# Kernel optimization log

Hardware: AMD Instinct MI355X
Metric: run time of the kernel (lower is better)

Reference implementation:

```python
import jax, jax.numpy as jnp
import numpy as np

EMBED_DIM = 512
NUM_HEADS = 8
HEAD_DIM = EMBED_DIM // NUM_HEADS
EDGE_DIM = 16
B, N = 2, 2048


def setup_inputs() -> dict:
    key = jax.random.key(0)
    ks = jax.random.split(key, 16)
    s = 1.0 / np.sqrt(EMBED_DIM)
    inp = {
        "x": jax.random.normal(ks[0], (B, N, EMBED_DIM), dtype=jnp.float32),
        "adjacency": jax.random.uniform(ks[1], (B, N, N), dtype=jnp.float32),
        # torch.nn.Linear stores weight as (out, in); we keep that convention
        "Wq": jax.random.uniform(ks[2], (EMBED_DIM, EMBED_DIM), minval=-s, maxval=s),
        "bq": jax.random.uniform(ks[3], (EMBED_DIM,), minval=-s, maxval=s),
        "Wk": jax.random.uniform(ks[4], (EMBED_DIM, EMBED_DIM), minval=-s, maxval=s),
        "bk": jax.random.uniform(ks[5], (EMBED_DIM,), minval=-s, maxval=s),
        "Wv": jax.random.uniform(ks[6], (EMBED_DIM, EMBED_DIM), minval=-s, maxval=s),
        "bv": jax.random.uniform(ks[7], (EMBED_DIM,), minval=-s, maxval=s),
        "Wo": jax.random.uniform(ks[8], (EMBED_DIM, EMBED_DIM), minval=-s, maxval=s),
        "bo": jax.random.uniform(ks[9], (EMBED_DIM,), minval=-s, maxval=s),
        # edge MLP: Linear(1 -> edge_dim) then Linear(edge_dim -> num_heads)
        "We1": jax.random.uniform(ks[10], (EDGE_DIM, 1), minval=-1.0, maxval=1.0),
        "be1": jax.random.uniform(ks[11], (EDGE_DIM,), minval=-1.0, maxval=1.0),
        "We2": jax.random.uniform(ks[12], (NUM_HEADS, EDGE_DIM), minval=-0.25, maxval=0.25),
        "be2": jax.random.uniform(ks[13], (NUM_HEADS,), minval=-0.25, maxval=0.25),
        "edge_bias": jnp.zeros((NUM_HEADS,), dtype=jnp.float32),
    }
    return inp


def reference(x, adjacency, Wq, bq, Wk, bk, Wv, bv, Wo, bo, We1, be1, We2, be2, edge_bias):
    b, n, _ = x.shape
    scale = HEAD_DIM ** (-0.5)

    def split_heads(t):  # (b, n, E) -> (b, H, n, d)
        return t.reshape(b, n, NUM_HEADS, HEAD_DIM).transpose(0, 2, 1, 3)

    q = split_heads(x @ Wq.T + bq)
    k = split_heads(x @ Wk.T + bk)
    v = split_heads(x @ Wv.T + bv)

    # (b, H, n, n)
    attn_scores = jnp.einsum('bhid,bhjd->bhij', q, k) * scale

    # edge MLP applied pointwise to each adjacency entry: 1 -> edge_dim -> num_heads
    # hidden: (b, n, n, edge_dim)
    hidden = jax.nn.relu(adjacency[..., None] * We1[:, 0] + be1)
    edge_attn = jnp.einsum('bijE,hE->bhij', hidden, We2) + be2[None, :, None, None]

    boost = adjacency[:, None, :, :] * edge_bias[None, :, None, None]
    attn_scores = attn_scores + edge_attn + boost

    attn_probs = jax.nn.softmax(attn_scores, axis=-1)
    out = jnp.einsum('bhij,bhjd->bhid', attn_probs, v)
    out = out.transpose(0, 2, 1, 3).reshape(b, n, EMBED_DIM)
    out = out @ Wo.T + bo
    return out
```

## Files before the change

### kernel.cpp

```cpp
#include <hip/hip_runtime.h>
#include <stdint.h>


#define SEQ 2048
#define EMB 512
#define NH  8
#define HD  64
#define NB  2
#define L2E 1.4426950408889634f

typedef unsigned int   u32;
typedef unsigned short u16;
typedef u32   u32x4  __attribute__((ext_vector_type(4)));
typedef float f32x4  __attribute__((ext_vector_type(4)));
typedef __bf16 bf16x8 __attribute__((ext_vector_type(8)));

#define MFMA16(a, b, c) __builtin_amdgcn_mfma_f32_16x16x32_bf16((a), (b), (c), 0, 0, 0)

static __device__ __forceinline__ u16 f2bf(float f) {
  return __builtin_bit_cast(u16, (__bf16)f);
}
static __device__ __forceinline__ u32 pack2(float a, float b) {
  return (u32)f2bf(a) | ((u32)f2bf(b) << 16);
}
static __device__ __forceinline__ bf16x8 ldfrag(const u16* p) {
  return __builtin_bit_cast(bf16x8, *(const u32x4*)p);
}


__global__ void prep_kernel(const float* __restrict__ x,
                            const float* __restrict__ Wq, const float* __restrict__ Wk,
                            const float* __restrict__ Wv, const float* __restrict__ Wo,
                            const float* __restrict__ We1, const float* __restrict__ be1,
                            const float* __restrict__ We2, const float* __restrict__ be2,
                            const float* __restrict__ ebias,
                            u16* __restrict__ xb, u16* __restrict__ wqkv,
                            u16* __restrict__ wob, float* __restrict__ co) {
  const int blk = blockIdx.x, tid = threadIdx.x;
  if (blk < 2048) {
    int i = (blk * 256 + tid) * 4;
    float4 v = *(const float4*)(x + i);
    *(uint2*)(xb + i) = make_uint2(pack2(v.x, v.y), pack2(v.z, v.w));
  } else if (blk < 3072) {
    int i = ((blk - 2048) * 256 + tid) * 4;
    int m = i >> 18;
    int off = i & 262143;
    const float* src = (m == 0) ? Wq : ((m == 1) ? Wk : ((m == 2) ? Wv : Wo));
    u16* dst = (m < 3) ? (wqkv + (size_t)m * 262144) : wob;
    float4 v = *(const float4*)(src + off);
    *(uint2*)(dst + off) = make_uint2(pack2(v.x, v.y), pack2(v.z, v.w));
  } else {
    const int e = tid & 15, h = tid >> 4;
    if (tid < 128) {
      co[49 + e * 8 + h] = 0.0f;
      if (h == 0) { co[17 + e] = 0.0f; co[33 + e] = 0.0f; }
    }
    __syncthreads();
    if (tid < 128) {
      float w1 = We1[e], b1 = be1[e], w2 = We2[h * 16 + e];
      float u0 = b1, u1 = w1 + b1;
      bool on  = (u0 >= 0.0f) && (u1 >= 0.0f);
      bool off = (u0 <= 0.0f) && (u1 <= 0.0f);
      bool crossing = (!on) && (!off);
      float ca = on ? (w2 * b1) : (crossing ? 0.5f * w2 * b1 : 0.0f);
      float cb = on ? (w2 * w1) : (crossing ? 0.5f * w2 * w1 : 0.0f);
      #pragma unroll
      for (int d = 1; d < 16; d <<= 1) { ca += __shfl_xor(ca, d); cb += __shfl_xor(cb, d); }
      if (e == 0) { co[h] = (be2[h] + ca) * L2E; co[8 + h] = (ebias[h] + cb) * L2E; }
      unsigned long long msk = __ballot(crossing);
      int midx = __popcll(msk & 0xFFFFull & ((1ull << e) - 1ull));
      int mcnt = __popcll(msk & 0xFFFFull);
      if (crossing) {
        co[49 + midx * 8 + h] = 0.5f * w2 * L2E;
        if (h == 0) { co[17 + midx] = w1; co[33 + midx] = b1; }
      }
      if (tid == 0) ((int*)co)[16] = mcnt;
    }
  }
}

#define LDA 40
__global__ __launch_bounds__(256) void gemm_qkv_kernel(
    const u16* __restrict__ A, const u16* __restrict__ Bm,
    const float* __restrict__ bq, const float* __restrict__ bk, const float* __restrict__ bv,
    u16* __restrict__ qh, u16* __restrict__ ksw, u16* __restrict__ vsw)
{
  __shared__ u16 As[64 * LDA];
  __shared__ u16 Bs[128 * LDA];
  const int tid = threadIdx.x;
  const int lane = tid & 63, w = tid >> 6;
  const int q = lane >> 4, l15 = lane & 15;
  const int m0 = blockIdx.y * 64;
  const int n0 = blockIdx.x * 128;

  f32x4 acc[4][2];
  f32x4 zero = {0.f, 0.f, 0.f, 0.f};
  #pragma unroll
  for (int i = 0; i < 4; i++) { acc[i][0] = zero; acc[i][1] = zero; }

  const bool isA = tid < 128;
  const int arow = tid >> 1, ahalf = tid & 1;
  const int brow = tid - 128;
  const u16* ga = A  + (size_t)(m0 + arow) * EMB + ahalf * 16;
  const u16* gb = Bm + (size_t)(n0 + brow) * EMB;
  u16* la = &As[arow * LDA + ahalf * 16];
  u16* lb = &Bs[brow * LDA];

  u32x4 p0, p1, p2, p3;
  if (isA) {
    p0 = *(const u32x4*)(ga); p1 = *(const u32x4*)(ga + 8); ga += 32;
  } else {
    p0 = *(const u32x4*)(gb);      p1 = *(const u32x4*)(gb + 8);
    p2 = *(const u32x4*)(gb + 16); p3 = *(const u32x4*)(gb + 24); gb += 32;
  }

  for (int k0 = 0; k0 < EMB; k0 += 32) {
    __syncthreads();
    if (isA) { *(u32x4*)(la) = p0; *(u32x4*)(la + 8) = p1; }
    else {
      *(u32x4*)(lb)      = p0; *(u32x4*)(lb + 8)  = p1;
      *(u32x4*)(lb + 16) = p2; *(u32x4*)(lb + 24) = p3;
    }
    __syncthreads();
    if (k0 + 32 < EMB) {
      if (isA) { p0 = *(const u32x4*)(ga); p1 = *(const u32x4*)(ga + 8); ga += 32; }
      else {
        p0 = *(const u32x4*)(gb);      p1 = *(const u32x4*)(gb + 8);
        p2 = *(const u32x4*)(gb + 16); p3 = *(const u32x4*)(gb + 24); gb += 32;
      }
    }
    bf16x8 af[4], bfr[2];
    #pragma unroll
    for (int mi = 0; mi < 4; mi++)
      af[mi] = ldfrag(&As[(mi*16 + l15) * LDA + q*8]);
    #pragma unroll
    for (int ni = 0; ni < 2; ni++)
      bfr[ni] = ldfrag(&Bs[(w*32 + ni*16 + l15) * LDA + q*8]);
    #pragma unroll
    for (int mi = 0; mi < 4; mi++)
      #pragma unroll
      for (int ni = 0; ni < 2; ni++)
        acc[mi][ni] = MFMA16(af[mi], bfr[ni], acc[mi][ni]);
  }

  const int mat = n0 >> 9;

  #pragma unroll
  for (int mi = 0; mi < 4; mi++) {
    int rowb = m0 + mi*16 + q*4;
    #pragma unroll
    for (int ni = 0; ni < 2; ni++) {
      int col = n0 + w*32 + ni*16 + l15;
      int oo = col & 511;
      int hh = oo >> 6, dd = oo & 63;
      if (mat == 0) {
        float bsv = bq[oo];
        #pragma unroll
        for (int r = 0; r < 4; r++) {
          int grow = rowb + r;
          int b_ = grow >> 11, n_ = grow & 2047;
          float val = (acc[mi][ni][r] + bsv) * (0.125f * L2E);
          qh[((size_t)(b_ * NH + hh) * SEQ + n_) * HD + dd] = f2bf(val);
        }
      } else if (mat == 1) {
        float bsv = bk[oo];
        #pragma unroll
        for (int r = 0; r < 4; r++) {
          int grow = rowb + r;
          int b_ = grow >> 11, n_ = grow & 2047;
          float val = acc[mi][ni][r] + bsv;
          size_t addr = (size_t)(b_ * NH + hh) * 131072
                      + (n_ >> 4) * 1024 + ((dd >> 5) << 9)
                      + ((((dd >> 3) & 3) * 16 + (n_ & 15)) << 3) + (dd & 7);
          ksw[addr] = f2bf(val);
        }
      } else {
        float bsv = bv[oo];
        #pragma unroll
        for (int r = 0; r < 4; r++) {
          int grow = rowb + r;
          int b_ = grow >> 11, n_ = grow & 2047;
          float val = acc[mi][ni][r] + bsv;
          size_t addr = (size_t)(b_ * NH + hh) * 131072
                      + (n_ >> 6) * 4096 + ((dd >> 4) << 10) + (((n_ >> 5) & 1) << 9)
                      + ((((n_ >> 3) & 3) * 16 + (dd & 15)) << 3) + (n_ & 7);
          vsw[addr] = f2bf(val);
        }
      }
    }
  }
}

__global__ __launch_bounds__(256) void gemm_out_kernel(
    const u16* __restrict__ A, const u16* __restrict__ Bm,
    const float* __restrict__ bo, float* __restrict__ out)
{
  __shared__ u16 As[64 * LDA];
  __shared__ u16 Bs[64 * LDA];
  const int tid = threadIdx.x;
  const int lane = tid & 63, w = tid >> 6;
  const int q = lane >> 4, l15 = lane & 15;
  const int m0 = blockIdx.y * 64;
  const int n0 = blockIdx.x * 64;

  f32x4 acc[4];
  f32x4 zero = {0.f, 0.f, 0.f, 0.f};
  #pragma unroll
  for (int i = 0; i < 4; i++) acc[i] = zero;

  const bool isA = tid < 128;
  const int row = isA ? (tid >> 1) : ((tid - 128) >> 1);
  const int half = tid & 1;
  const u16* g = (isA ? A + (size_t)(m0 + row) * EMB : Bm + (size_t)(n0 + row) * EMB)
               + half * 16;
  u16* l = (isA ? &As[row * LDA] : &Bs[row * LDA]) + half * 16;

  u32x4 p0 = *(const u32x4*)(g);
  u32x4 p1 = *(const u32x4*)(g + 8);
  g += 32;

  for (int k0 = 0; k0 < EMB; k0 += 32) {
    __syncthreads();
    *(u32x4*)(l) = p0; *(u32x4*)(l + 8) = p1;
    __syncthreads();
    if (k0 + 32 < EMB) {
      p0 = *(const u32x4*)(g); p1 = *(const u32x4*)(g + 8); g += 32;
    }
    bf16x8 af[4], bfr;
    #pragma unroll
    for (int mi = 0; mi < 4; mi++)
      af[mi] = ldfrag(&As[(mi*16 + l15) * LDA + q*8]);
    bfr = ldfrag(&Bs[(w*16 + l15) * LDA + q*8]);
    #pragma unroll
    for (int mi = 0; mi < 4; mi++)
      acc[mi] = MFMA16(af[mi], bfr, acc[mi]);
  }

  int col = n0 + w*16 + l15;
  float bsv = bo[col];
  #pragma unroll
  for (int mi = 0; mi < 4; mi++) {
    int rowb = m0 + mi*16 + q*4;
    #pragma unroll
    for (int r = 0; r < 4; r++)
      out[(size_t)(rowb + r) * EMB + col] = acc[mi][r] + bsv;
  }
}

template<int MT>
__device__ __forceinline__ void flash_body(
    u16* __restrict__ smem,
    const u16* __restrict__ qh, const u16* __restrict__ ksw, const u16* __restrict__ vsw,
    const float* __restrict__ adj, const float* __restrict__ coeff, u16* __restrict__ om)
{
  const int tid = threadIdx.x, lane = tid & 63, w = tid >> 6;
  const int q = lane >> 4, l15 = lane & 15;
  const int i0 = blockIdx.x * 64;
  const int h = blockIdx.y, b = blockIdx.z;
  const int bh = b * NH + h;
  const int iw = i0 + (w & 3) * 16;
  const int jbase = (w >> 2) * 1024;

  const float Ah = coeff[h], Bh = coeff[8 + h];
  float ctr[MT], dtr[MT], wtr[MT];
  #pragma unroll
  for (int t = 0; t < MT; t++) {
    ctr[t] = coeff[17 + t];
    dtr[t] = coeff[33 + t];
    wtr[t] = coeff[49 + t * 8 + h];
  }

  const u16* qrow = qh + ((size_t)bh * SEQ + iw + l15) * HD;
  bf16x8 qf0 = ldfrag(qrow + q * 8);
  bf16x8 qf1 = ldfrag(qrow + 32 + q * 8);

  const u16* kbase = ksw + (size_t)bh * 131072 + jbase * 64 + lane * 8;
  const u16* vbase = vsw + (size_t)bh * 131072 + jbase * 64 + lane * 8;
  const float* arow = adj + ((size_t)b * SEQ + iw + l15) * SEQ + jbase + q * 4;

  f32x4 O[4];
  f32x4 zero = {0.f, 0.f, 0.f, 0.f};
  #pragma unroll
  for (int dt = 0; dt < 4; dt++) O[dt] = zero;
  float lsum = 0.0f;

  u16* psw = smem + w * 16 * 72;

  for (int it = 0; it < 16; it++) {
    const int off = it * 4096;

    bf16x8 kf[8];
    #pragma unroll
    for (int jt = 0; jt < 4; jt++) {
      kf[jt*2]   = ldfrag(kbase + off + jt * 1024);
      kf[jt*2+1] = ldfrag(kbase + off + jt * 1024 + 512);
    }
    float4 av[4];
    #pragma unroll
    for (int jt = 0; jt < 4; jt++)
      av[jt] = *(const float4*)(arow + it * 64 + jt * 16);

    f32x4 S[4];
    #pragma unroll
    for (int jt = 0; jt < 4; jt++) {
      f32x4 s = MFMA16(kf[jt*2], qf0, zero);
      S[jt] = MFMA16(kf[jt*2+1], qf1, s);
    }

    bf16x8 vf[8];
    #pragma unroll
    for (int dt = 0; dt < 4; dt++) {
      vf[dt*2]   = ldfrag(vbase + off + dt * 1024);
      vf[dt*2+1] = ldfrag(vbase + off + dt * 1024 + 512);
    }

    #pragma unroll
    for (int jt = 0; jt < 4; jt++) {
      float p[4];
      #pragma unroll
      for (int r = 0; r < 4; r++) {
        float a = ((const float*)&av[jt])[r];
        float e = fmaf(a, Bh, Ah);
        #pragma unroll
        for (int t = 0; t < MT; t++)
          e = fmaf(fabsf(fmaf(a, ctr[t], dtr[t])), wtr[t], e);
        p[r] = __builtin_amdgcn_exp2f(S[jt][r] + e);
        lsum += p[r];
      }
      *(uint2*)(psw + l15 * 72 + jt * 16 + q * 4) =
          make_uint2(pack2(p[0], p[1]), pack2(p[2], p[3]));
    }

    bf16x8 pf0 = ldfrag(psw + l15 * 72 + q * 8);
    bf16x8 pf1 = ldfrag(psw + l15 * 72 + 32 + q * 8);
    #pragma unroll
    for (int dt = 0; dt < 4; dt++) {
      O[dt] = MFMA16(vf[dt*2],   pf0, O[dt]);
      O[dt] = MFMA16(vf[dt*2+1], pf1, O[dt]);
    }
  }

  lsum += __shfl_xor(lsum, 16);
  lsum += __shfl_xor(lsum, 32);

  __syncthreads();
  float* fbuf = (float*)smem;
  if (w >= 4) {
    int bi = ((w & 3) * 64 + lane) * 17;
    #pragma unroll
    for (int dt = 0; dt < 4; dt++)
      #pragma unroll
      for (int r = 0; r < 4; r++) fbuf[bi + dt * 4 + r] = O[dt][r];
    fbuf[bi + 16] = lsum;
  }
  __syncthreads();
  if (w < 4) {
    int bi = (w * 64 + lane) * 17;
    float rl = 1.0f / (lsum + fbuf[bi + 16]);
    u16* orow = om + ((size_t)b * SEQ + iw + l15) * EMB + h * HD + q * 4;
    #pragma unroll
    for (int dt = 0; dt < 4; dt++) {
      float v0 = (O[dt][0] + fbuf[bi + dt * 4 + 0]) * rl;
      float v1 = (O[dt][1] + fbuf[bi + dt * 4 + 1]) * rl;
      float v2 = (O[dt][2] + fbuf[bi + dt * 4 + 2]) * rl;
      float v3 = (O[dt][3] + fbuf[bi + dt * 4 + 3]) * rl;
      *(uint2*)(orow + dt * 16) = make_uint2(pack2(v0, v1), pack2(v2, v3));
    }
  }
}

__global__ __launch_bounds__(512, 4) void flash_kernel(
    const u16* __restrict__ qh, const u16* __restrict__ ksw, const u16* __restrict__ vsw,
    const float* __restrict__ adj, const float* __restrict__ coeff, u16* __restrict__ om)
{
  __shared__ __align__(16) u16 smem[8 * 16 * 72];
  const int mt = ((const int*)coeff)[16];
  if (mt <= 4)      flash_body<4>(smem, qh, ksw, vsw, adj, coeff, om);
  else if (mt <= 8) flash_body<8>(smem, qh, ksw, vsw, adj, coeff, om);
  else              flash_body<16>(smem, qh, ksw, vsw, adj, coeff, om);
}

extern "C" void kernel_launch(void* const* d_in, const int* in_sizes, int n_in,
                              void* d_out, int out_size, void* d_ws, size_t ws_size,
                              hipStream_t stream) {
  const float* x     = (const float*)d_in[0];
  const float* adj   = (const float*)d_in[1];
  const float* Wq    = (const float*)d_in[2];
  const float* bq    = (const float*)d_in[3];
  const float* Wk    = (const float*)d_in[4];
  const float* bk    = (const float*)d_in[5];
  const float* Wv    = (const float*)d_in[6];
  const float* bv    = (const float*)d_in[7];
  const float* Wo    = (const float*)d_in[8];
  const float* bo    = (const float*)d_in[9];
  const float* We1   = (const float*)d_in[10];
  const float* be1   = (const float*)d_in[11];
  const float* We2   = (const float*)d_in[12];
  const float* be2   = (const float*)d_in[13];
  const float* ebias = (const float*)d_in[14];
  float* out = (float*)d_out;

  char* ws = (char*)d_ws;
  u16*   xb   = (u16*)(ws + 0);
  u16*   wqkv = (u16*)(ws + 4194304);
  u16*   wob  = (u16*)(ws + 5767168);
  u16*   qh   = (u16*)(ws + 6291456);
  u16*   ksw  = (u16*)(ws + 10485760);
  u16*   vsw  = (u16*)(ws + 14680064);
  u16*   om   = (u16*)(ws + 18874368);
  float* co   = (float*)(ws + 23068672);
  if (ws_size < 23069696) return;

  prep_kernel<<<3073, 256, 0, stream>>>(x, Wq, Wk, Wv, Wo, We1, be1, We2, be2, ebias,
                                        xb, wqkv, wob, co);
  gemm_qkv_kernel<<<dim3(12, 64), 256, 0, stream>>>(xb, wqkv, bq, bk, bv, qh, ksw, vsw);
  flash_kernel<<<dim3(32, NH, NB), 512, 0, stream>>>(qh, ksw, vsw, adj, co, om);
  gemm_out_kernel<<<dim3(8, 64), 256, 0, stream>>>(om, wob, bo, out);
}
```

Baseline: 208.2 us.

## Stage QKV epilogue through LDS and prefetch K/adjacency in flash loop

The QKV GEMM epilogue now writes each head's 64x64 tile into shared memory in the target swizzled layout and then copies it out with coalesced 16-byte stores, replacing scattered 2-byte global writes. The flash kernel drops the split-K scheme across 8 waves and the LDS reduction that went with it. Each block now has 4 waves that each walk the full key range of 32 steps. K fragments and adjacency values for the next step are software-prefetched while the current step computes. This trades block-level parallelism and occupancy (launch bounds 256,3) for less reduction overhead and better latency hiding.

```diff
diff --git a/kernel.cpp b/kernel.cpp
--- a/kernel.cpp
+++ b/kernel.cpp
@@ -85,8 +85,9 @@
     const float* __restrict__ bq, const float* __restrict__ bk, const float* __restrict__ bv,
     u16* __restrict__ qh, u16* __restrict__ ksw, u16* __restrict__ vsw)
 {
-  __shared__ u16 As[64 * LDA];
-  __shared__ u16 Bs[128 * LDA];
+  __shared__ u16 sm[64 * LDA + 128 * LDA];
+  u16* As = sm;
+  u16* Bs = sm + 64 * LDA;
   const int tid = threadIdx.x;
   const int lane = tid & 63, w = tid >> 6;
   const int q = lane >> 4, l15 = lane & 15;
@@ -99,11 +100,11 @@
   for (int i = 0; i < 4; i++) { acc[i][0] = zero; acc[i][1] = zero; }
 
   const bool isA = tid < 128;
-  const int arow = tid >> 1, ahalf = tid & 1;
+  const int arow_ = tid >> 1, ahalf = tid & 1;
   const int brow = tid - 128;
-  const u16* ga = A  + (size_t)(m0 + arow) * EMB + ahalf * 16;
+  const u16* ga = A  + (size_t)(m0 + arow_) * EMB + ahalf * 16;
   const u16* gb = Bm + (size_t)(n0 + brow) * EMB;
-  u16* la = &As[arow * LDA + ahalf * 16];
+  u16* la = &As[arow_ * LDA + ahalf * 16];
   u16* lb = &Bs[brow * LDA];
 
   u32x4 p0, p1, p2, p3;
@@ -144,50 +145,44 @@
   }
 
   const int mat = n0 >> 9;
-
-  #pragma unroll
-  for (int mi = 0; mi < 4; mi++) {
-    int rowb = m0 + mi*16 + q*4;
-    #pragma unroll
-    for (int ni = 0; ni < 2; ni++) {
-      int col = n0 + w*32 + ni*16 + l15;
-      int oo = col & 511;
-      int hh = oo >> 6, dd = oo & 63;
-      if (mat == 0) {
-        float bsv = bq[oo];
+  const float* bias = (mat == 0) ? bq : ((mat == 1) ? bk : bv);
+  const float mul = (mat == 0) ? 0.125f * L2E : 1.0f;
+  const int b_ = m0 >> 11;
+  const int nbase = m0 & 2047;
+
+  #pragma unroll
+  for (int p = 0; p < 2; p++) {
+    __syncthreads();
+    if ((w >> 1) == p) {
+      #pragma unroll
+      for (int ni = 0; ni < 2; ni++) {
+        const int dd = (w & 1) * 32 + ni * 16 + l15;
+        const float bsv = bias[(n0 & 511) + (w * 32 + ni * 16 + l15)];
         #pragma unroll
-        for (int r = 0; r < 4; r++) {
-          int grow = rowb + r;
-          int b_ = grow >> 11, n_ = grow & 2047;
-          float val = (acc[mi][ni][r] + bsv) * (0.125f * L2E);
-          qh[((size_t)(b_ * NH + hh) * SEQ + n_) * HD + dd] = f2bf(val);
-        }
-      } else if (mat == 1) {
-        float bsv = bk[oo];
-        #pragma unroll
-        for (int r = 0; r < 4; r++) {
-          int grow = rowb + r;
-          int b_ = grow >> 11, n_ = grow & 2047;
-          float val = acc[mi][ni][r] + bsv;
-          size_t addr = (size_t)(b_ * NH + hh) * 131072
-                      + (n_ >> 4) * 1024 + ((dd >> 5) << 9)
-                      + ((((dd >> 3) & 3) * 16 + (n_ & 15)) << 3) + (dd & 7);
-          ksw[addr] = f2bf(val);
-        }
-      } else {
-        float bsv = bv[oo];
-        #pragma unroll
-        for (int r = 0; r < 4; r++) {
-          int grow = rowb + r;
-          int b_ = grow >> 11, n_ = grow & 2047;
-          float val = acc[mi][ni][r] + bsv;
-          size_t addr = (size_t)(b_ * NH + hh) * 131072
-                      + (n_ >> 6) * 4096 + ((dd >> 4) << 10) + (((n_ >> 5) & 1) << 9)
-                      + ((((n_ >> 3) & 3) * 16 + (dd & 15)) << 3) + (n_ & 7);
-          vsw[addr] = f2bf(val);
+        for (int mi = 0; mi < 4; mi++) {
+          #pragma unroll
+          for (int r = 0; r < 4; r++) {
+            const int nr = mi * 16 + q * 4 + r;
+            const float val = (acc[mi][ni][r] + bsv) * mul;
+            int idx;
+            if (mat == 0)      idx = nr * 64 + dd;
+            else if (mat == 1) idx = (nr >> 4) * 1024 + ((dd >> 5) << 9)
+                                   + ((((dd >> 3) & 3) * 16 + (nr & 15)) << 3) + (dd & 7);
+            else               idx = ((dd >> 4) << 10) + (((nr >> 5) & 1) << 9)
+                                   + ((((nr >> 3) & 3) * 16 + (dd & 15)) << 3) + (nr & 7);
+            sm[idx] = f2bf(val);
+          }
         }
       }
     }
+    __syncthreads();
+    const int hh = ((n0 & 511) >> 6) + p;
+    u16* gdst;
+    if (mat == 0)      gdst = qh  + ((size_t)(b_ * NH + hh) * SEQ + nbase) * HD;
+    else if (mat == 1) gdst = ksw + (size_t)(b_ * NH + hh) * 131072 + (nbase >> 4) * 1024;
+    else               gdst = vsw + (size_t)(b_ * NH + hh) * 131072 + (nbase >> 6) * 4096;
+    *(u32x4*)(gdst + tid * 16)     = *(const u32x4*)(sm + tid * 16);
+    *(u32x4*)(gdst + tid * 16 + 8) = *(const u32x4*)(sm + tid * 16 + 8);
   }
 }
 
@@ -258,8 +253,7 @@
   const int i0 = blockIdx.x * 64;
   const int h = blockIdx.y, b = blockIdx.z;
   const int bh = b * NH + h;
-  const int iw = i0 + (w & 3) * 16;
-  const int jbase = (w >> 2) * 1024;
+  const int iw = i0 + w * 16;
 
   const float Ah = coeff[h], Bh = coeff[8 + h];
   float ctr[MT], dtr[MT], wtr[MT];
@@ -274,9 +268,9 @@
   bf16x8 qf0 = ldfrag(qrow + q * 8);
   bf16x8 qf1 = ldfrag(qrow + 32 + q * 8);
 
-  const u16* kbase = ksw + (size_t)bh * 131072 + jbase * 64 + lane * 8;
-  const u16* vbase = vsw + (size_t)bh * 131072 + jbase * 64 + lane * 8;
-  const float* arow = adj + ((size_t)b * SEQ + iw + l15) * SEQ + jbase + q * 4;
+  const u16* kbase = ksw + (size_t)bh * 131072 + lane * 8;
+  const u16* vbase = vsw + (size_t)bh * 131072 + lane * 8;
+  const float* arow = adj + ((size_t)b * SEQ + iw + l15) * SEQ + q * 4;
 
   f32x4 O[4];
   f32x4 zero = {0.f, 0.f, 0.f, 0.f};
@@ -286,19 +280,27 @@
 
   u16* psw = smem + w * 16 * 72;
 
-  for (int it = 0; it < 16; it++) {
+  bf16x8 kf[8];
+  float4 av[4];
+  #pragma unroll
+  for (int jt = 0; jt < 4; jt++) {
+    kf[jt*2]   = ldfrag(kbase + jt * 1024);
+    kf[jt*2+1] = ldfrag(kbase + jt * 1024 + 512);
+    av[jt] = *(const float4*)(arow + jt * 16);
+  }
+
+  #pragma unroll 1
+  for (int it = 0; it < 32; it++) {
     const int off = it * 4096;
-
-    bf16x8 kf[8];
-    #pragma unroll
-    for (int jt = 0; jt < 4; jt++) {
-      kf[jt*2]   = ldfrag(kbase + off + jt * 1024);
-      kf[jt*2+1] = ldfrag(kbase + off + jt * 1024 + 512);
-    }
-    float4 av[4];
-    #pragma unroll
-    for (int jt = 0; jt < 4; jt++)
-      av[jt] = *(const float4*)(arow + it * 64 + jt * 16);
+    const int nx = (it + 1 < 32) ? it + 1 : 31;
+    const int noff = nx * 4096;
+
+    bf16x8 vf[8];
+    #pragma unroll
+    for (int dt = 0; dt < 2; dt++) {
+      vf[dt*2]   = ldfrag(vbase + off + dt * 1024);
+      vf[dt*2+1] = ldfrag(vbase + off + dt * 1024 + 512);
+    }
 
     f32x4 S[4];
     #pragma unroll
@@ -307,9 +309,13 @@
       S[jt] = MFMA16(kf[jt*2+1], qf1, s);
     }
 
-    bf16x8 vf[8];
-    #pragma unroll
-    for (int dt = 0; dt < 4; dt++) {
+    #pragma unroll
+    for (int jt = 0; jt < 4; jt++) {
+      kf[jt*2]   = ldfrag(kbase + noff + jt * 1024);
+      kf[jt*2+1] = ldfrag(kbase + noff + jt * 1024 + 512);
+    }
+    #pragma unroll
+    for (int dt = 2; dt < 4; dt++) {
       vf[dt*2]   = ldfrag(vbase + off + dt * 1024);
       vf[dt*2+1] = ldfrag(vbase + off + dt * 1024 + 512);
     }
@@ -327,6 +333,7 @@
         p[r] = __builtin_amdgcn_exp2f(S[jt][r] + e);
         lsum += p[r];
       }
+      av[jt] = *(const float4*)(arow + nx * 64 + jt * 16);
       *(uint2*)(psw + l15 * 72 + jt * 16 + q * 4) =
           make_uint2(pack2(p[0], p[1]), pack2(p[2], p[3]));
     }
@@ -342,38 +349,22 @@
 
   lsum += __shfl_xor(lsum, 16);
   lsum += __shfl_xor(lsum, 32);
-
-  __syncthreads();
-  float* fbuf = (float*)smem;
-  if (w >= 4) {
-    int bi = ((w & 3) * 64 + lane) * 17;
-    #pragma unroll
-    for (int dt = 0; dt < 4; dt++)
-      #pragma unroll
-      for (int r = 0; r < 4; r++) fbuf[bi + dt * 4 + r] = O[dt][r];
-    fbuf[bi + 16] = lsum;
-  }
-  __syncthreads();
-  if (w < 4) {
-    int bi = (w * 64 + lane) * 17;
-    float rl = 1.0f / (lsum + fbuf[bi + 16]);
-    u16* orow = om + ((size_t)b * SEQ + iw + l15) * EMB + h * HD + q * 4;
-    #pragma unroll
-    for (int dt = 0; dt < 4; dt++) {
-      float v0 = (O[dt][0] + fbuf[bi + dt * 4 + 0]) * rl;
-      float v1 = (O[dt][1] + fbuf[bi + dt * 4 + 1]) * rl;
-      float v2 = (O[dt][2] + fbuf[bi + dt * 4 + 2]) * rl;
-      float v3 = (O[dt][3] + fbuf[bi + dt * 4 + 3]) * rl;
-      *(uint2*)(orow + dt * 16) = make_uint2(pack2(v0, v1), pack2(v2, v3));
-    }
-  }
-}
-
-__global__ __launch_bounds__(512, 4) void flash_kernel(
+  float rl = 1.0f / lsum;
+
+  u16* orow = om + ((size_t)b * SEQ + iw + l15) * EMB + h * HD + q * 4;
+  #pragma unroll
+  for (int dt = 0; dt < 4; dt++) {
+    float v0 = O[dt][0] * rl, v1 = O[dt][1] * rl;
+    float v2 = O[dt][2] * rl, v3 = O[dt][3] * rl;
+    *(uint2*)(orow + dt * 16) = make_uint2(pack2(v0, v1), pack2(v2, v3));
+  }
+}
+
+__global__ __launch_bounds__(256, 3) void flash_kernel(
     const u16* __restrict__ qh, const u16* __restrict__ ksw, const u16* __restrict__ vsw,
     const float* __restrict__ adj, const float* __restrict__ coeff, u16* __restrict__ om)
 {
-  __shared__ __align__(16) u16 smem[8 * 16 * 72];
+  __shared__ __align__(16) u16 smem[4 * 16 * 72];
   const int mt = ((const int*)coeff)[16];
   if (mt <= 4)      flash_body<4>(smem, qh, ksw, vsw, adj, coeff, om);
   else if (mt <= 8) flash_body<8>(smem, qh, ksw, vsw, adj, coeff, om);
@@ -414,6 +405,6 @@
   prep_kernel<<<3073, 256, 0, stream>>>(x, Wq, Wk, Wv, Wo, We1, be1, We2, be2, ebias,
                                         xb, wqkv, wob, co);
   gemm_qkv_kernel<<<dim3(12, 64), 256, 0, stream>>>(xb, wqkv, bq, bk, bv, qh, ksw, vsw);
-  flash_kernel<<<dim3(32, NH, NB), 512, 0, stream>>>(qh, ksw, vsw, adj, co, om);
+  flash_kernel<<<dim3(32, NH, NB), 256, 0, stream>>>(qh, ksw, vsw, adj, co, om);
   gemm_out_kernel<<<dim3(8, 64), 256, 0, stream>>>(om, wob, bo, out);
 }
```

After: 201.0 us. -3.4%, faster.
